# Performance work log

Measured on AMD Instinct MI355X. Metric: run time of the kernel, lower is better.

## Reference

```python
import jax, jax.numpy as jnp
import numpy as np

NP_, NL_, ND_ = 100_000, 10_000, 500
E1, E2 = 2_000_000, 500_000
H, OUT = 128, 10
EPS = 1e-5


def setup_inputs() -> dict:
    key = jax.random.key(0)
    ks = jax.random.split(key, 20)
    n = lambda i, shape, s=1.0: jax.random.normal(ks[i], shape, jnp.float32) * s
    return {
        "x_patient": n(0, (NP_, 16)),
        "x_lab": n(1, (NL_, 1)),
        "x_disease": n(2, (ND_, 2)),
        "Wp": n(3, (16, H), 0.1), "bp": jnp.zeros(H),
        "Wlab": n(4, (1, H), 0.1), "blab": jnp.zeros(H),
        "Wdis": n(5, (2, H), 0.1), "bdis": jnp.zeros(H),
        "Wl1": n(6, (4, H, H), 0.05), "bl1": jnp.zeros((4, H)), "Wr1": n(7, (4, H, H), 0.05),
        "Wl2": n(8, (4, H, H), 0.05), "bl2": jnp.zeros((4, H)), "Wr2": n(9, (4, H, H), 0.05),
        "bn1_g": jnp.ones((3, H)), "bn1_b": jnp.zeros((3, H)),
        "bn2_g": jnp.ones((3, H)), "bn2_b": jnp.zeros((3, H)),
        "fc1_W": n(10, (H, H // 2), 0.1), "fc1_b": jnp.zeros(H // 2),
        "fc2_W": n(11, (H // 2, OUT), 0.1), "fc2_b": jnp.zeros(OUT),
        "e_haslab_src": jax.random.randint(ks[12], (E1,), 0, NP_, jnp.int32),
        "e_haslab_dst": jax.random.randint(ks[13], (E1,), 0, NL_, jnp.int32),
        "e_hasdis_src": jax.random.randint(ks[14], (E2,), 0, NP_, jnp.int32),
        "e_hasdis_dst": jax.random.randint(ks[15], (E2,), 0, ND_, jnp.int32),
    }


def _sage(x_src, x_dst, src, dst, n_dst, Wl, bl, Wr):
    # PyG SAGEConv: lin_l(mean_{j in N(i)} x_j) + lin_r(x_i); bias only on lin_l.
    agg = jax.ops.segment_sum(x_src[src], dst, num_segments=n_dst)  # [n_dst, H]
    cnt = jax.ops.segment_sum(jnp.ones(dst.shape, jnp.float32), dst, num_segments=n_dst)
    mean = agg / jnp.maximum(cnt, 1.0)[:, None]
    return mean @ Wl + bl + x_dst @ Wr


def _bn(x, g, b):
    # training-mode BatchNorm1d (biased variance), eps=1e-5
    m = x.mean(0)
    v = jnp.mean((x - m) ** 2, axis=0)
    return (x - m) * jax.lax.rsqrt(v + EPS) * g + b


def _hetero_layer(hp, hl, hd, s1, d1, s2, d2, Wl, bl, Wr, bn_g, bn_b):
    # edge-type order: 0 has_lab, 1 has_disease, 2 rev_has_lab, 3 rev_has_disease
    out_lab = _sage(hp, hl, s1, d1, NL_, Wl[0], bl[0], Wr[0])
    out_dis = _sage(hp, hd, s2, d2, ND_, Wl[1], bl[1], Wr[1])
    out_pat = (_sage(hl, hp, d1, s1, NP_, Wl[2], bl[2], Wr[2])
               + _sage(hd, hp, d2, s2, NP_, Wl[3], bl[3], Wr[3]))  # HeteroConv aggr='sum'
    hp = jax.nn.relu(_bn(out_pat, bn_g[0], bn_b[0]))
    hl = jax.nn.relu(_bn(out_lab, bn_g[1], bn_b[1]))
    hd = jax.nn.relu(_bn(out_dis, bn_g[2], bn_b[2]))
    return hp, hl, hd


def reference(x_patient, x_lab, x_disease, Wp, bp, Wlab, blab, Wdis, bdis,
              Wl1, bl1, Wr1, Wl2, bl2, Wr2, bn1_g, bn1_b, bn2_g, bn2_b,
              fc1_W, fc1_b, fc2_W, fc2_b,
              e_haslab_src, e_haslab_dst, e_hasdis_src, e_hasdis_dst):
    hp = x_patient @ Wp + bp
    hl = x_lab @ Wlab + blab
    hd = x_disease @ Wdis + bdis
    hp, hl, hd = _hetero_layer(hp, hl, hd, e_haslab_src, e_haslab_dst,
                               e_hasdis_src, e_hasdis_dst, Wl1, bl1, Wr1, bn1_g, bn1_b)
    hp, hl, hd = _hetero_layer(hp, hl, hd, e_haslab_src, e_haslab_dst,
                               e_hasdis_src, e_hasdis_dst, Wl2, bl2, Wr2, bn2_g, bn2_b)
    x = jax.nn.relu(hp @ fc1_W + fc1_b)
    x = x @ fc2_W + fc2_b
    return jax.nn.log_softmax(x, axis=1)
```

## Files before the change

kernel.cpp:

```cpp
#include <hip/hip_runtime.h>
#include <hip/hip_bf16.h>

#define NP 100000
#define NL 10000
#define ND 500
#define H 128
#define HH (H * H)
#define E1 2000000
#define E2 500000
#define EP (E1 + E2)
#define NOUT 10
#define NCNT (NL + ND + 2 * NP)
#define NROW (NL + ND)
#define CHUNK 8192
#define LABHB ((E1 + CHUNK - 1) / CHUNK)
#define DISHB ((E2 + CHUNK - 1) / CHUNK)
#define CNT_BLOCKS ((E1 + E2 + 255) / 256)
#define RED_LAB ((NL + 255) / 256)
#define RED_DIS ((ND + 255) / 256)
#define PAT_BLOCKS (NP / 16)

#define CHP 15625
#define NCH1 (E1 / CHP)
#define NCH2 (E2 / CHP)
#define NPW (NP / 4)
#define RPW ((NPW + 255) / 256)

typedef __hip_bfloat16 bf16;
typedef __attribute__((ext_vector_type(8))) short bf16x8;
typedef __attribute__((ext_vector_type(4))) float f32x4;

__device__ __forceinline__ float bfbits2f(unsigned short s) {
    union { unsigned int u; float f; } v;
    v.u = (unsigned int)s << 16;
    return v.f;
}
__device__ __forceinline__ float2 ld_bf2(const bf16* p) {
    unsigned int u = *(const unsigned int*)p;
    return make_float2(bfbits2f((unsigned short)(u & 0xFFFFu)), bfbits2f((unsigned short)(u >> 16)));
}
__device__ __forceinline__ float2 ld_bf2_nt(const bf16* p) {
    unsigned int u = __builtin_nontemporal_load((const unsigned int*)p);
    return make_float2(bfbits2f((unsigned short)(u & 0xFFFFu)), bfbits2f((unsigned short)(u >> 16)));
}
__device__ __forceinline__ void st_bf2(bf16* p, float2 v) {
    union { unsigned int u; bf16 b[2]; } t;
    t.b[0] = __float2bfloat16(v.x);
    t.b[1] = __float2bfloat16(v.y);
    *(unsigned int*)p = t.u;
}
__device__ __forceinline__ float ldin(const void* p, size_t i, int f32m) {
    return f32m ? ((const float*)p)[i] : __bfloat162float(((const bf16*)p)[i]);
}
__device__ __forceinline__ void bfacc2(float& x, float& y, unsigned int u) {
    union { unsigned int q; float f; } lo, hi;
    lo.q = u << 16;
    hi.q = u & 0xFFFF0000u;
    x += lo.f;
    y += hi.f;
}

#define HB0 NCH1
#define HB1 (HB0 + NCH2)
#define HB2 (HB1 + LABHB)
#define HB3 (HB2 + DISHB)
__global__ void k_hist(const int* __restrict__ e1s, const int* __restrict__ e1d,
                       const int* __restrict__ e2s, const int* __restrict__ e2d,
                       unsigned int* __restrict__ labHistP, unsigned int* __restrict__ disHistP,
                       unsigned char* __restrict__ r1s, unsigned char* __restrict__ r2s,
                       unsigned int* __restrict__ labHist, unsigned int* __restrict__ disHist,
                       const unsigned short* __restrict__ xpw, int* __restrict__ flags) {
    __shared__ unsigned int sh[NPW];
    int b = blockIdx.x, t = threadIdx.x;
    if (b < HB1) {
        for (int i = t; i < NPW; i += 1024) sh[i] = 0;
        __syncthreads();
        if (b < HB0) {
            int e0 = b * CHP;
            for (int j = t; j < CHP; j += 1024) {
                int e = e0 + j;
                int ss = e1s[e];
                unsigned int old = atomicAdd(&sh[ss >> 2], 1u << (8 * (ss & 3)));
                r1s[e] = (unsigned char)(old >> (8 * (ss & 3)));
            }
            __syncthreads();
            unsigned int* out = labHistP + (size_t)b * NPW;
            for (int i = t; i < NPW; i += 1024) out[i] = sh[i];
        } else {
            int c = b - HB0;
            int e0 = c * CHP;
            for (int j = t; j < CHP; j += 1024) {
                int e = e0 + j;
                int ss = e2s[e];
                unsigned int old = atomicAdd(&sh[ss >> 2], 1u << (8 * (ss & 3)));
                r2s[e] = (unsigned char)(old >> (8 * (ss & 3)));
            }
            __syncthreads();
            unsigned int* out = disHistP + (size_t)c * NPW;
            for (int i = t; i < NPW; i += 1024) out[i] = sh[i];
        }
    } else if (b < HB2) {
        int c = b - HB1;
        for (int i = t; i < NL / 2; i += 1024) sh[i] = 0;
        __syncthreads();
        int e0 = c * CHUNK, ee = min(E1, e0 + CHUNK);
        for (int e = e0 + t; e < ee; e += 1024) {
            int dd = e1d[e];
            atomicAdd(&sh[dd >> 1], 1u << (16 * (dd & 1)));
        }
        __syncthreads();
        for (int i = t; i < NL; i += 1024)
            labHist[(size_t)c * NL + i] = (sh[i >> 1] >> (16 * (i & 1))) & 0xFFFFu;
    } else if (b < HB3) {
        int c = b - HB2;
        for (int i = t; i < ND / 2; i += 1024) sh[i] = 0;
        __syncthreads();
        int e0 = c * CHUNK, ee = min(E2, e0 + CHUNK);
        for (int e = e0 + t; e < ee; e += 1024) {
            int dd = e2d[e];
            atomicAdd(&sh[dd >> 1], 1u << (16 * (dd & 1)));
        }
        __syncthreads();
        for (int i = t; i < ND; i += 1024)
            disHist[(size_t)c * ND + i] = (sh[i >> 1] >> (16 * (i & 1))) & 0xFFFFu;
    } else {
        int cnt = 0;
        for (int i = t; i < 4096; i += 1024) {
            unsigned short w = xpw[2 * i];
            int e = (w >> 7) & 0xFF;
            if (w == 0 || (e >= 114 && e <= 141)) cnt++;
        }
        int* shi = (int*)sh;
        shi[t] = cnt;
        __syncthreads();
        for (int s = 512; s > 0; s >>= 1) {
            if (t < s) shi[t] += shi[t + s];
            __syncthreads();
        }
        if (t == 0) flags[0] = (shi[0] < 2048) ? 1 : 0;
    }
}

#define EMB2 ((NP + 255) / 256)
#define RB0 RED_LAB
#define RB1 (RB0 + RED_DIS)
#define RB2 (RB1 + RPW)
#define RB3 (RB2 + RPW)
#define RB4 (RB3 + EMB2)
#define RB5 (RB4 + 16)
#define RB6 (RB5 + 7)
#define RB7 (RB6 + 64)
__global__ void k_reduce(unsigned int* __restrict__ labHist, unsigned int* __restrict__ disHist,
                         unsigned int* __restrict__ labHistP, unsigned int* __restrict__ disHistP,
                         int* __restrict__ cnt, const void* __restrict__ xp,
                         const void* __restrict__ Wp, const void* __restrict__ bp,
                         const void* __restrict__ Wlab, const void* __restrict__ blab,
                         const void* __restrict__ Wdis, const void* __restrict__ bdis,
                         const void* __restrict__ Wl1, const void* __restrict__ bl1,
                         const void* __restrict__ Wr1, bf16* __restrict__ hp,
                         float* __restrict__ WpWl0, float* __restrict__ WpWl1,
                         float* __restrict__ vecs, bf16* __restrict__ w23bT1,
                         bf16* __restrict__ xpb, const int* __restrict__ flags) {
    int b = blockIdx.x, t = threadIdx.x;
    if (b < RB0) {
        int bin = b * 256 + t;
        if (bin < NL) {
            unsigned int run = 0;
            for (int k = 0; k < LABHB; ++k) {
                unsigned int x = labHist[(size_t)k * NL + bin];
                labHist[(size_t)k * NL + bin] = run;
                run += x;
            }
            cnt[bin] = (int)run;
        }
    } else if (b < RB1) {
        int bin = (b - RB0) * 256 + t;
        if (bin < ND) {
            unsigned int run = 0;
            for (int k = 0; k < DISHB; ++k) {
                unsigned int x = disHist[(size_t)k * ND + bin];
                disHist[(size_t)k * ND + bin] = run;
                run += x;
            }
            cnt[NL + bin] = (int)run;
        }
    } else if (b < RB2) {
        int w = (b - RB1) * 256 + t;
        if (w < NPW) {
            unsigned int run = 0;
            for (int c = 0; c < NCH1; ++c) {
                unsigned int x = labHistP[(size_t)c * NPW + w];
                labHistP[(size_t)c * NPW + w] = run;
                run += x;
            }
            int base = NL + ND + 4 * w;
            cnt[base] = (int)(run & 0xFFu);
            cnt[base + 1] = (int)((run >> 8) & 0xFFu);
            cnt[base + 2] = (int)((run >> 16) & 0xFFu);
            cnt[base + 3] = (int)(run >> 24);
        }
    } else if (b < RB3) {
        int w = (b - RB2) * 256 + t;
        if (w < NPW) {
            unsigned int run = 0;
            for (int c = 0; c < NCH2; ++c) {
                unsigned int x = disHistP[(size_t)c * NPW + w];
                disHistP[(size_t)c * NPW + w] = run;
                run += x;
            }
            int base = NL + ND + NP + 4 * w;
            cnt[base] = (int)(run & 0xFFu);
            cnt[base + 1] = (int)((run >> 8) & 0xFFu);
            cnt[base + 2] = (int)((run >> 16) & 0xFFu);
            cnt[base + 3] = (int)(run >> 24);
        }
    } else if (b < RB4) {
        __shared__ float Wps[16 * 128];
        __shared__ float bps[128];
        int f32m = flags[0];
        for (int i = t; i < 16 * 128; i += 256) Wps[i] = ldin(Wp, i, f32m);
        if (t < 128) bps[t] = ldin(bp, t, f32m);
        __syncthreads();
        int p = (b - RB3) * 256 + t;
        if (p < NP) {
            float xr[16];
#pragma unroll
            for (int k = 0; k < 16; ++k) xr[k] = ldin(xp, (size_t)p * 16 + k, f32m);
            unsigned int xw[8];
#pragma unroll
            for (int k2 = 0; k2 < 8; ++k2) {
                union { unsigned int u; bf16 b2[2]; } tt;
                tt.b2[0] = __float2bfloat16(xr[2 * k2]);
                tt.b2[1] = __float2bfloat16(xr[2 * k2 + 1]);
                xw[k2] = tt.u;
            }
            *(uint4*)(xpb + (size_t)p * 16) = make_uint4(xw[0], xw[1], xw[2], xw[3]);
            *(uint4*)(xpb + (size_t)p * 16 + 8) = make_uint4(xw[4], xw[5], xw[6], xw[7]);
            bf16* hrow = hp + (size_t)p * H;
            for (int hc = 0; hc < 16; ++hc) {
                unsigned int ow[4];
#pragma unroll
                for (int hh = 0; hh < 8; hh += 2) {
                    int h0 = hc * 8 + hh;
                    float a0 = bps[h0], a1 = bps[h0 + 1];
#pragma unroll
                    for (int k = 0; k < 16; ++k) {
                        a0 = fmaf(xr[k], Wps[k * 128 + h0], a0);
                        a1 = fmaf(xr[k], Wps[k * 128 + h0 + 1], a1);
                    }
                    union { unsigned int u; bf16 b2[2]; } tt;
                    tt.b2[0] = __float2bfloat16(a0);
                    tt.b2[1] = __float2bfloat16(a1);
                    ow[hh >> 1] = tt.u;
                }
                *(uint4*)(hrow + hc * 8) = make_uint4(ow[0], ow[1], ow[2], ow[3]);
            }
        }
    } else if (b < RB5) {
        int f32m = flags[0];
        int pb = b - RB4;
        bool first = pb < 8;
        size_t woff = first ? 0 : (size_t)HH;
        float* outp = first ? WpWl0 : WpWl1;
        int k = (first ? pb : pb - 8) * 2 + (t >> 7);
        int h = t & 127;
        float s = 0.f;
        for (int m = 0; m < H; ++m)
            s = fmaf(ldin(Wp, (size_t)k * H + m, f32m), ldin(Wl1, woff + (size_t)m * H + h, f32m), s);
        outp[k * H + h] = s;
    } else if (b < RB6) {
        int f32m = flags[0];
        int idx = (b - RB5) * 256 + t;
        if (idx < 13 * 128) {
            int v = idx >> 7, h = idx & 127;
            float s = 0.f;
            if (v == 12) {
                s = ldin(bl1, 2 * H + h, f32m) + ldin(bl1, 3 * H + h, f32m);
            } else {
                const void* A;
                size_t aoff = 0;
                const void* W;
                size_t woff;
                float add = 0.f;
                switch (v) {
                    case 0: A = Wlab; W = Wl1; woff = 2 * (size_t)HH; break;
                    case 1: A = blab; W = Wl1; woff = 2 * (size_t)HH; break;
                    case 2: A = Wdis; W = Wl1; woff = 3 * (size_t)HH; break;
                    case 3: A = Wdis; aoff = H; W = Wl1; woff = 3 * (size_t)HH; break;
                    case 4: A = bdis; W = Wl1; woff = 3 * (size_t)HH; break;
                    case 5: A = Wlab; W = Wr1; woff = 0; break;
                    case 6: A = blab; W = Wr1; woff = 0; add = ldin(bl1, h, f32m); break;
                    case 7: A = Wdis; W = Wr1; woff = (size_t)HH; break;
                    case 8: A = Wdis; aoff = H; W = Wr1; woff = (size_t)HH; break;
                    case 9: A = bdis; W = Wr1; woff = (size_t)HH; add = ldin(bl1, H + h, f32m); break;
                    case 10: A = bp; W = Wl1; woff = 0; break;
                    default: A = bp; W = Wl1; woff = (size_t)HH; break;
                }
                for (int m = 0; m < H; ++m)
                    s = fmaf(ldin(A, aoff + m, f32m), ldin(W, woff + (size_t)m * H + h, f32m), s);
                s += add;
            }
            vecs[v * 128 + h] = s;
        }
    } else {
        int f32m = flags[0];
        int idx = (b - RB6) * 256 + t;
        if (idx < HH) {
            int k = idx >> 7, n = idx & 127;
            float v = ldin(Wr1, (size_t)2 * HH + idx, f32m) + ldin(Wr1, (size_t)3 * HH + idx, f32m);
            w23bT1[(size_t)n * H + k] = __float2bfloat16(v);
        }
    }
}

#define SCAN_ELEMS 2048
__global__ void k_scan1(const int* __restrict__ in, int* __restrict__ out,
                        int* __restrict__ bsums, int n) {
    int t = threadIdx.x;
    int base = blockIdx.x * SCAN_ELEMS + t * 8;
    int v[8], tsum = 0;
#pragma unroll
    for (int j = 0; j < 8; ++j) {
        v[j] = (base + j < n) ? in[base + j] : 0;
        tsum += v[j];
    }
    __shared__ int sh[256];
    sh[t] = tsum;
    __syncthreads();
    for (int d = 1; d < 256; d <<= 1) {
        int x = (t >= d) ? sh[t - d] : 0;
        __syncthreads();
        sh[t] += x;
        __syncthreads();
    }
    int run = sh[t] - tsum;
    if (t == 255) bsums[blockIdx.x] = sh[255];
#pragma unroll
    for (int j = 0; j < 8; ++j) {
        if (base + j < n) out[base + j] = run;
        run += v[j];
    }
}

__global__ void k_scan2(int* __restrict__ bsums, int nb) {
    int t = threadIdx.x;
    int v = (t < nb) ? bsums[t] : 0;
    __shared__ int sh[256];
    sh[t] = v;
    __syncthreads();
    for (int d = 1; d < 256; d <<= 1) {
        int x = (t >= d) ? sh[t - d] : 0;
        __syncthreads();
        sh[t] += x;
        __syncthreads();
    }
    if (t < nb) bsums[t] = sh[t] - v;
}

__global__ void k_scan3(int* __restrict__ out, const int* __restrict__ bsums, int n) {
    int i = blockIdx.x * 256 + threadIdx.x;
    if (i < n) out[i] += bsums[i / SCAN_ELEMS];
}

__global__ void k_fill(const int* __restrict__ e1s, const int* __restrict__ e1d,
                       const int* __restrict__ e2s, const int* __restrict__ e2d,
                       const int* __restrict__ off, const unsigned char* __restrict__ r1s,
                       const unsigned char* __restrict__ r2s,
                       const unsigned char* __restrict__ labBase,
                       const unsigned char* __restrict__ disBase,
                       const unsigned int* __restrict__ labHist,
                       const unsigned int* __restrict__ disHist, int* __restrict__ nbr,
                       unsigned short* __restrict__ nbrP, float* __restrict__ bns) {
    __shared__ unsigned int slot[NL];
    int b = blockIdx.x, t = threadIdx.x;
    if (b < CNT_BLOCKS) {
        int e = b * 256 + t;
        if (e < E1) {
            int ss = e1s[e];
            int c = e / CHP;
            int pos = off[NL + ND + ss] + (int)labBase[(size_t)c * NP + ss] + (int)r1s[e] - EP;
            nbrP[pos] = (unsigned short)e1d[e];
        } else if (e < E1 + E2) {
            int i = e - E1;
            int ss = e2s[i];
            int c = i / CHP;
            int pos = off[NL + ND + NP + ss] + (int)disBase[(size_t)c * NP + ss] + (int)r2s[i] - EP;
            nbrP[pos] = (unsigned short)e2d[i];
        }
    } else if (b < CNT_BLOCKS + LABHB) {
        int c = b - CNT_BLOCKS;
        for (int i = t; i < NL; i += 256)
            slot[i] = (unsigned int)off[i] + labHist[(size_t)c * NL + i];
        __syncthreads();
        int e0 = c * CHUNK, ee = min(E1, e0 + CHUNK);
        for (int e = e0 + t; e < ee; e += 256) {
            unsigned int pos = atomicAdd(&slot[e1d[e]], 1u);
            nbr[pos] = e1s[e];
        }
    } else if (b < CNT_BLOCKS + LABHB + DISHB) {
        int c = b - CNT_BLOCKS - LABHB;
        for (int i = t; i < ND; i += 256)
            slot[i] = (unsigned int)off[NL + i] + disHist[(size_t)c * ND + i];
        __syncthreads();
        int e0 = c * CHUNK, ee = min(E2, e0 + CHUNK);
        for (int e = e0 + t; e < ee; e += 256) {
            unsigned int pos = atomicAdd(&slot[e2d[e]], 1u);
            nbr[pos] = e2s[e];
        }
    } else {
        for (int i = t; i < 8 * H; i += 256) bns[i] = 0.f;
    }
}

__global__ void k_stage1_L1(const bf16* __restrict__ xpb, const int* __restrict__ off,
                            const int* __restrict__ cnt, const int* __restrict__ nbr,
                            float* __restrict__ mxp) {
    __shared__ float red[4][64][16];
    int t = threadIdx.x;
    int w = t >> 6, lane = t & 63;
    int row = blockIdx.x * 4 + w;
    float acc[16];
#pragma unroll
    for (int d = 0; d < 16; ++d) acc[d] = 0.f;
    if (row < NROW) {
        int s0 = off[row], c = cnt[row];
        const int* nb = nbr + s0;
        int j = lane;
        for (; j + 64 < c; j += 128) {
            int p0 = nb[j], p1 = nb[j + 64];
            const uint4* r0 = (const uint4*)(xpb + (size_t)p0 * 16);
            const uint4* r1 = (const uint4*)(xpb + (size_t)p1 * 16);
            uint4 u0 = r0[0], u1 = r0[1];
            uint4 v0 = r1[0], v1 = r1[1];
            bfacc2(acc[0], acc[1], u0.x);   bfacc2(acc[2], acc[3], u0.y);
            bfacc2(acc[4], acc[5], u0.z);   bfacc2(acc[6], acc[7], u0.w);
            bfacc2(acc[8], acc[9], u1.x);   bfacc2(acc[10], acc[11], u1.y);
            bfacc2(acc[12], acc[13], u1.z); bfacc2(acc[14], acc[15], u1.w);
            bfacc2(acc[0], acc[1], v0.x);   bfacc2(acc[2], acc[3], v0.y);
            bfacc2(acc[4], acc[5], v0.z);   bfacc2(acc[6], acc[7], v0.w);
            bfacc2(acc[8], acc[9], v1.x);   bfacc2(acc[10], acc[11], v1.y);
            bfacc2(acc[12], acc[13], v1.z); bfacc2(acc[14], acc[15], v1.w);
        }
        if (j < c) {
            const uint4* r0 = (const uint4*)(xpb + (size_t)nb[j] * 16);
            uint4 u0 = r0[0], u1 = r0[1];
            bfacc2(acc[0], acc[1], u0.x);   bfacc2(acc[2], acc[3], u0.y);
            bfacc2(acc[4], acc[5], u0.z);   bfacc2(acc[6], acc[7], u0.w);
            bfacc2(acc[8], acc[9], u1.x);   bfacc2(acc[10], acc[11], u1.y);
            bfacc2(acc[12], acc[13], u1.z); bfacc2(acc[14], acc[15], u1.w);
        }
    }
#pragma unroll
    for (int d = 0; d < 16; ++d) red[w][lane][d] = acc[d];
    __syncthreads();
    if (t < 64) {
        int w2 = t >> 4, d = t & 15;
        int row2 = blockIdx.x * 4 + w2;
        if (row2 < NROW) {
            float s = 0.f;
#pragma unroll 8
            for (int l = 0; l < 64; ++l) s += red[w2][l][d];
            mxp[(size_t)row2 * 16 + d] = s / fmaxf((float)cnt[row2], 1.f);
        }
    }
}

#define LD1_BLOCKS ((NROW + 1) / 2)
#define HPAD 136
#define APAD 132
__global__ void k_patmm_L1(const bf16* __restrict__ hp, const void* __restrict__ xl,
                           const void* __restrict__ xd, const int* __restrict__ off,
                           const int* __restrict__ cnt, const unsigned short* __restrict__ nbrP,
                           const bf16* __restrict__ w23bT1, const float* __restrict__ vecs,
                           const float* __restrict__ WpWl0, const float* __restrict__ WpWl1,
                           const float* __restrict__ mxp, bf16* __restrict__ aggp,
                           float* __restrict__ bufL, float* __restrict__ bufD,
                           float* __restrict__ blocksums, const int* __restrict__ flags) {
    int t = threadIdx.x;
    int f32m = flags[0];
    if (blockIdx.x < PAT_BLOCKS) {
        __shared__ bf16 hpA[16][HPAD];
        __shared__ float accf[16][APAD];
        __shared__ float svec[6][128];
        __shared__ float s_mxl[16], s_onL[16], s_d0[16], s_d1[16], s_onD[16];
        int w = t >> 6, lane = t & 63;
        int p0 = blockIdx.x * 16;
        {
            const unsigned int* hpu = (const unsigned int*)(hp + (size_t)p0 * H);
            for (int i = t; i < 16 * 64; i += 256) {
                int r = i >> 6, c = i & 63;
                *(unsigned int*)&hpA[r][2 * c] = hpu[(size_t)r * 64 + c];
            }
        }
        {
            const int map[6] = {0, 1, 2, 3, 4, 12};
            for (int i = t; i < 6 * 128; i += 256)
                svec[i >> 7][i & 127] = vecs[map[i >> 7] * 128 + (i & 127)];
        }
        {
            int g = t >> 4, sl = t & 15;
            int p = p0 + g;
            int s1 = off[NL + ND + p] - EP, c1 = cnt[NL + ND + p];
            float a = 0.f;
            for (int j = sl; j < c1; j += 16) a += ldin(xl, nbrP[s1 + j], f32m);
            a += __shfl_xor(a, 1);
            a += __shfl_xor(a, 2);
            a += __shfl_xor(a, 4);
            a += __shfl_xor(a, 8);
            int s2 = off[NL + ND + NP + p] - EP, c2 = cnt[NL + ND + NP + p];
            float d0 = 0.f, d1 = 0.f;
            for (int j = sl; j < c2; j += 16) {
                int q = nbrP[s2 + j];
                d0 += ldin(xd, (size_t)2 * q, f32m);
                d1 += ldin(xd, (size_t)2 * q + 1, f32m);
            }
            d0 += __shfl_xor(d0, 1); d0 += __shfl_xor(d0, 2);
            d0 += __shfl_xor(d0, 4); d0 += __shfl_xor(d0, 8);
            d1 += __shfl_xor(d1, 1); d1 += __shfl_xor(d1, 2);
            d1 += __shfl_xor(d1, 4); d1 += __shfl_xor(d1, 8);
            if (sl == 0) {
                s_mxl[g] = a / fmaxf((float)c1, 1.f);
                s_onL[g] = (c1 > 0) ? 1.f : 0.f;
                s_d0[g] = d0 / fmaxf((float)c2, 1.f);
                s_d1[g] = d1 / fmaxf((float)c2, 1.f);
                s_onD[g] = (c2 > 0) ? 1.f : 0.f;
            }
        }
        __syncthreads();
        {
            int m = lane & 15, kg = lane >> 4;
            bf16x8 afr[4];
#pragma unroll
            for (int ks = 0; ks < 4; ++ks)
                afr[ks] = *(const bf16x8*)&hpA[m][ks * 32 + kg * 8];
            int n0 = w * 32;
#pragma unroll
            for (int tt = 0; tt < 2; ++tt) {
                int nc = n0 + tt * 16 + m;
                f32x4 acc = {0.f, 0.f, 0.f, 0.f};
#pragma unroll
                for (int ks = 0; ks < 4; ++ks) {
                    bf16x8 bfr = *(const bf16x8*)&w23bT1[(size_t)nc * H + ks * 32 + kg * 8];
                    acc = __builtin_amdgcn_mfma_f32_16x16x32_bf16(afr[ks], bfr, acc, 0, 0, 0);
                }
#pragma unroll
                for (int rg = 0; rg < 4; ++rg)
                    accf[kg * 4 + rg][nc] = acc[rg];
            }
        }
        __syncthreads();
        for (int i = t; i < 16 * 64; i += 256) {
            int r = i >> 6, cc = (i & 63) * 2;
            float l0 = s_onL[r] * fmaf(s_mxl[r], svec[0][cc], svec[1][cc]);
            float l1 = s_onL[r] * fmaf(s_mxl[r], svec[0][cc + 1], svec[1][cc + 1]);
            float q0 = s_onD[r] * (s_d0[r] * svec[2][cc] + s_d1[r] * svec[3][cc] + svec[4][cc]);
            float q1 = s_onD[r] * (s_d0[r] * svec[2][cc + 1] + s_d1[r] * svec[3][cc + 1] + svec[4][cc + 1]);
            float v0 = accf[r][cc] + l0 + q0 + svec[5][cc];
            float v1 = accf[r][cc + 1] + l1 + q1 + svec[5][cc + 1];
            accf[r][cc] = v0;
            accf[r][cc + 1] = v1;
            st_bf2(aggp + (size_t)(p0 + r) * H + cc, make_float2(v0, v1));
        }
        __syncthreads();
        if (t < 128) {
            float s = 0.f, q = 0.f;
#pragma unroll
            for (int r = 0; r < 16; ++r) {
                float v = accf[r][t];
                s += v;
                q = fmaf(v, v, q);
            }
            blocksums[(size_t)blockIdx.x * 256 + t] = s;
            blocksums[(size_t)blockIdx.x * 256 + 128 + t] = q;
        }
    } else {
        int bb = blockIdx.x - PAT_BLOCKS;
        int rr = bb * 2 + (t >> 7);
        int h = t & 127;
        if (rr >= NROW) return;
        if (rr < NL) {
            float acc = vecs[6 * 128 + h] + ldin(xl, rr, f32m) * vecs[5 * 128 + h];
            if (cnt[rr] > 0) {
                float s = vecs[10 * 128 + h];
                const float* mx = mxp + (size_t)rr * 16;
#pragma unroll
                for (int k = 0; k < 16; ++k) s = fmaf(mx[k], WpWl0[k * H + h], s);
                acc += s;
            }
            bufL[(size_t)rr * H + h] = acc;
        } else {
            int rd = rr - NL;
            float acc = vecs[9 * 128 + h] + ldin(xd, (size_t)2 * rd, f32m) * vecs[7 * 128 + h] +
                        ldin(xd, (size_t)2 * rd + 1, f32m) * vecs[8 * 128 + h];
            if (cnt[rr] > 0) {
                float s = vecs[11 * 128 + h];
                const float* mx = mxp + (size_t)rr * 16;
#pragma unroll
                for (int k = 0; k < 16; ++k) s = fmaf(mx[k], WpWl1[k * H + h], s);
                acc += s;
            }
            bufD[(size_t)rd * H + h] = acc;
        }
    }
}

__global__ void k_bnred(const float* __restrict__ blocksums, const float* __restrict__ bufL,
                        const float* __restrict__ bufD, float* __restrict__ sums) {
    int b = blockIdx.x, t = threadIdx.x;
    if (b < 64) {
        float acc = 0.f;
        for (int r = b; r < PAT_BLOCKS; r += 64) acc += blocksums[(size_t)r * 256 + t];
        atomicAdd(&sums[t], acc);
        return;
    }
    int h = t & 127;
    int sub = t >> 7;
    float s = 0.f, s2 = 0.f;
    float* sm;
    if (b < 320) {
        int bid = b - 64;
        for (int i = bid * 2 + sub; i < NL; i += 512) {
            float v = bufL[(size_t)i * H + h];
            s += v;
            s2 = fmaf(v, v, s2);
        }
        sm = sums + 2 * H;
    } else {
        int bid = b - 320;
        for (int i = bid * 2 + sub; i < ND; i += 128) {
            float v = bufD[(size_t)i * H + h];
            s += v;
            s2 = fmaf(v, v, s2);
        }
        sm = sums + 4 * H;
    }
    __shared__ float ls[256], ls2[256];
    ls[t] = s;
    ls2[t] = s2;
    __syncthreads();
    if (sub == 0) {
        atomicAdd(&sm[h], s + ls[128 + h]);
        atomicAdd(&sm[H + h], s2 + ls2[128 + h]);
    }
}

#define S2_MM 1313
#define S2_PREP 64
#define S2_TOTAL (S2_MM + S2_PREP)
__global__ void k_stage1_L2(const float* __restrict__ bufL, const float* __restrict__ bufD,
                            const float* __restrict__ bns, const void* __restrict__ bng1,
                            const void* __restrict__ bnb1, const void* __restrict__ Wl,
                            bf16* __restrict__ tlp, bf16* __restrict__ tdp,
                            const void* __restrict__ Wr, const void* __restrict__ bl,
                            bf16* __restrict__ w23bT, float* __restrict__ b23,
                            const void* __restrict__ W1in, bf16* __restrict__ w1T,
                            const int* __restrict__ flags) {
    __shared__ float smm[8][H];
    int b = blockIdx.x, t = threadIdx.x;
    int f32m = flags[0];
    if (b < S2_MM) {
        int bb = b;
        bool lab = bb < 1250;
        const float* buf = lab ? bufL : bufD;
        int N = lab ? NL : ND;
        float invN = lab ? 1.f / NL : 1.f / ND;
        int so = lab ? 2 * H : 4 * H;
        int go = lab ? H : 2 * H;
        bf16* outp = lab ? tlp : tdp;
        size_t woff = lab ? (size_t)2 * HH : (size_t)3 * HH;
        int r0 = (lab ? bb : bb - 1250) * 8;
        int h = t & 127, half = t >> 7;
        float m = bns[so + h] * invN;
        float v = fmaf(-m, m, bns[so + H + h] * invN);
        float sc = rsqrtf(v + 1e-5f) * ldin(bng1, go + h, f32m);
        float be = ldin(bnb1, go + h, f32m);
        for (int r = half; r < 8; r += 2) {
            int ri = r0 + r;
            float x = (ri < N) ? buf[(size_t)ri * H + h] : 0.f;
            smm[r][h] = (ri < N) ? fmaxf(fmaf(x - m, sc, be), 0.f) : 0.f;
        }
        __syncthreads();
        int rb = half * 4;
        float a0 = 0.f, a1 = 0.f, a2 = 0.f, a3 = 0.f;
        for (int k = 0; k < H; ++k) {
            float wv = ldin(Wl, woff + (size_t)k * H + h, f32m);
            a0 = fmaf(smm[rb + 0][k], wv, a0);
            a1 = fmaf(smm[rb + 1][k], wv, a1);
            a2 = fmaf(smm[rb + 2][k], wv, a2);
            a3 = fmaf(smm[rb + 3][k], wv, a3);
        }
        float acc[4] = {a0, a1, a2, a3};
#pragma unroll
        for (int r = 0; r < 4; ++r)
            if (r0 + rb + r < N)
                outp[(size_t)(r0 + rb + r) * H + h] = __float2bfloat16(acc[r]);
    } else {
        int pb = b - S2_MM;
        int idx = pb * 256 + t;
        if (idx < HH) {
            int k = idx >> 7, n = idx & 127;
            float v = ldin(Wr, (size_t)2 * HH + idx, f32m) + ldin(Wr, (size_t)3 * HH + idx, f32m);
            w23bT[(size_t)n * H + k] = __float2bfloat16(v);
        }
        if (idx < H)
            b23[idx] = ldin(bl, (size_t)2 * H + idx, f32m) + ldin(bl, (size_t)3 * H + idx, f32m);
        if (idx < 64 * H) {
            int n = idx >> 7, k = idx & 127;
            w1T[idx] = __float2bfloat16(ldin(W1in, (size_t)k * 64 + n, f32m));
        }
    }
}

__global__ void k_patmm_L2(bf16* __restrict__ aggp, const bf16* __restrict__ tlp,
                           const bf16* __restrict__ tdp, const int* __restrict__ off,
                           const int* __restrict__ cnt, const unsigned short* __restrict__ nbrP,
                           const bf16* __restrict__ w23bT, const float* __restrict__ b23,
                           const float* __restrict__ bns, const void* __restrict__ bng1,
                           const void* __restrict__ bnb1, float* __restrict__ blocksums,
                           const int* __restrict__ flags) {
    __shared__ bf16 hpA[16][HPAD];
    __shared__ __align__(16) float accf[16][APAD];
    int t = threadIdx.x;
    int f32m = flags[0];
    int w = t >> 6, lane = t & 63;
    int p0 = blockIdx.x * 16;
    {
        int cc = (t & 63) * 2;
        const float invN = 1.f / NP;
        float m0 = bns[cc] * invN, m1 = bns[cc + 1] * invN;
        float v0 = fmaf(-m0, m0, bns[128 + cc] * invN);
        float v1 = fmaf(-m1, m1, bns[128 + cc + 1] * invN);
        float sc0 = rsqrtf(v0 + 1e-5f) * ldin(bng1, cc, f32m);
        float sc1 = rsqrtf(v1 + 1e-5f) * ldin(bng1, cc + 1, f32m);
        float be0 = ldin(bnb1, cc, f32m), be1 = ldin(bnb1, cc + 1, f32m);
        for (int i = t; i < 16 * 64; i += 256) {
            int r = i >> 6;
            float2 v = ld_bf2_nt(aggp + (size_t)(p0 + r) * H + cc);
            st_bf2(&hpA[r][cc], make_float2(fmaxf(fmaf(v.x - m0, sc0, be0), 0.f),
                                            fmaxf(fmaf(v.y - m1, sc1, be1), 0.f)));
        }
    }
    {
        const int* off1 = off + NL + ND;
        const int* cnt1 = cnt + NL + ND;
        const int* off2 = off + NL + ND + NP;
        const int* cnt2 = cnt + NL + ND + NP;
        int qw = lane >> 4, ql = lane & 15;
        int p = p0 + w * 4 + qw;
        int cb = ql * 8;
        float4 bb0 = *(const float4*)(b23 + cb);
        float4 bb1 = *(const float4*)(b23 + cb + 4);
        int s1 = off1[p] - EP, c1 = cnt1[p];
        const unsigned short* nb1 = nbrP + s1;
        float a0 = 0.f, a1 = 0.f, a2 = 0.f, a3 = 0.f, a4 = 0.f, a5 = 0.f, a6 = 0.f, a7 = 0.f;
        float g0 = 0.f, g1 = 0.f, g2 = 0.f, g3 = 0.f, g4 = 0.f, g5 = 0.f, g6 = 0.f, g7 = 0.f;
        int j = 0;
        int i0, i1, i2, i3;
        if (c1 >= 4) { i0 = nb1[0]; i1 = nb1[1]; i2 = nb1[2]; i3 = nb1[3]; }
        for (; j + 8 <= c1; j += 4) {
            uint4 v0 = *(const uint4*)(tlp + (size_t)i0 * H + cb);
            uint4 v1 = *(const uint4*)(tlp + (size_t)i1 * H + cb);
            uint4 v2 = *(const uint4*)(tlp + (size_t)i2 * H + cb);
            uint4 v3 = *(const uint4*)(tlp + (size_t)i3 * H + cb);
            int n0 = nb1[j + 4], n1 = nb1[j + 5], n2 = nb1[j + 6], n3 = nb1[j + 7];
            bfacc2(a0, a1, v0.x); bfacc2(a2, a3, v0.y); bfacc2(a4, a5, v0.z); bfacc2(a6, a7, v0.w);
            bfacc2(g0, g1, v1.x); bfacc2(g2, g3, v1.y); bfacc2(g4, g5, v1.z); bfacc2(g6, g7, v1.w);
            bfacc2(a0, a1, v2.x); bfacc2(a2, a3, v2.y); bfacc2(a4, a5, v2.z); bfacc2(a6, a7, v2.w);
            bfacc2(g0, g1, v3.x); bfacc2(g2, g3, v3.y); bfacc2(g4, g5, v3.z); bfacc2(g6, g7, v3.w);
            i0 = n0; i1 = n1; i2 = n2; i3 = n3;
        }
        if (j + 4 <= c1) {
            uint4 v0 = *(const uint4*)(tlp + (size_t)i0 * H + cb);
            uint4 v1 = *(const uint4*)(tlp + (size_t)i1 * H + cb);
            uint4 v2 = *(const uint4*)(tlp + (size_t)i2 * H + cb);
            uint4 v3 = *(const uint4*)(tlp + (size_t)i3 * H + cb);
            bfacc2(a0, a1, v0.x); bfacc2(a2, a3, v0.y); bfacc2(a4, a5, v0.z); bfacc2(a6, a7, v0.w);
            bfacc2(g0, g1, v1.x); bfacc2(g2, g3, v1.y); bfacc2(g4, g5, v1.z); bfacc2(g6, g7, v1.w);
            bfacc2(a0, a1, v2.x); bfacc2(a2, a3, v2.y); bfacc2(a4, a5, v2.z); bfacc2(a6, a7, v2.w);
            bfacc2(g0, g1, v3.x); bfacc2(g2, g3, v3.y); bfacc2(g4, g5, v3.z); bfacc2(g6, g7, v3.w);
            j += 4;
        }
        for (; j < c1; ++j) {
            uint4 v = *(const uint4*)(tlp + (size_t)nb1[j] * H + cb);
            bfacc2(a0, a1, v.x); bfacc2(a2, a3, v.y); bfacc2(a4, a5, v.z); bfacc2(a6, a7, v.w);
        }
        a0 += g0; a1 += g1; a2 += g2; a3 += g3;
        a4 += g4; a5 += g5; a6 += g6; a7 += g7;
        int s2 = off2[p] - EP, c2 = cnt2[p];
        const unsigned short* nb2 = nbrP + s2;
        float d0 = 0.f, d1 = 0.f, d2 = 0.f, d3 = 0.f, d4 = 0.f, d5 = 0.f, d6 = 0.f, d7 = 0.f;
        float e0 = 0.f, e1 = 0.f, e2 = 0.f, e3 = 0.f, e4 = 0.f, e5 = 0.f, e6 = 0.f, e7 = 0.f;
        j = 0;
        int k0, k1;
        if (c2 >= 2) { k0 = nb2[0]; k1 = nb2[1]; }
        for (; j + 4 <= c2; j += 2) {
            uint4 v0 = *(const uint4*)(tdp + (size_t)k0 * H + cb);
            uint4 v1 = *(const uint4*)(tdp + (size_t)k1 * H + cb);
            int n0 = nb2[j + 2], n1 = nb2[j + 3];
            bfacc2(d0, d1, v0.x); bfacc2(d2, d3, v0.y); bfacc2(d4, d5, v0.z); bfacc2(d6, d7, v0.w);
            bfacc2(e0, e1, v1.x); bfacc2(e2, e3, v1.y); bfacc2(e4, e5, v1.z); bfacc2(e6, e7, v1.w);
            k0 = n0; k1 = n1;
        }
        if (j + 2 <= c2) {
            uint4 v0 = *(const uint4*)(tdp + (size_t)k0 * H + cb);
            uint4 v1 = *(const uint4*)(tdp + (size_t)k1 * H + cb);
            bfacc2(d0, d1, v0.x); bfacc2(d2, d3, v0.y); bfacc2(d4, d5, v0.z); bfacc2(d6, d7, v0.w);
            bfacc2(e0, e1, v1.x); bfacc2(e2, e3, v1.y); bfacc2(e4, e5, v1.z); bfacc2(e6, e7, v1.w);
            j += 2;
        }
        if (j < c2) {
            uint4 v = *(const uint4*)(tdp + (size_t)nb2[j] * H + cb);
            bfacc2(d0, d1, v.x); bfacc2(d2, d3, v.y); bfacc2(d4, d5, v.z); bfacc2(d6, d7, v.w);
        }
        d0 += e0; d1 += e1; d2 += e2; d3 += e3;
        d4 += e4; d5 += e5; d6 += e6; d7 += e7;
        float i1f = 1.f / fmaxf((float)c1, 1.f), i2f = 1.f / fmaxf((float)c2, 1.f);
        float4 r0v, r1v;
        r0v.x = a0 * i1f + d0 * i2f + bb0.x;
        r0v.y = a1 * i1f + d1 * i2f + bb0.y;
        r0v.z = a2 * i1f + d2 * i2f + bb0.z;
        r0v.w = a3 * i1f + d3 * i2f + bb0.w;
        r1v.x = a4 * i1f + d4 * i2f + bb1.x;
        r1v.y = a5 * i1f + d5 * i2f + bb1.y;
        r1v.z = a6 * i1f + d6 * i2f + bb1.z;
        r1v.w = a7 * i1f + d7 * i2f + bb1.w;
        *(float4*)&accf[w * 4 + qw][cb] = r0v;
        *(float4*)&accf[w * 4 + qw][cb + 4] = r1v;
    }
    __syncthreads();
    {
        int m = lane & 15, kg = lane >> 4;
        bf16x8 afr[4];
#pragma unroll
        for (int ks = 0; ks < 4; ++ks)
            afr[ks] = *(const bf16x8*)&hpA[m][ks * 32 + kg * 8];
        int n0 = w * 32;
#pragma unroll
        for (int tt = 0; tt < 2; ++tt) {
            int nc = n0 + tt * 16 + m;
            f32x4 acc = {0.f, 0.f, 0.f, 0.f};
#pragma unroll
            for (int ks = 0; ks < 4; ++ks) {
                bf16x8 bfr = *(const bf16x8*)&w23bT[(size_t)nc * H + ks * 32 + kg * 8];
                acc = __builtin_amdgcn_mfma_f32_16x16x32_bf16(afr[ks], bfr, acc, 0, 0, 0);
            }
#pragma unroll
            for (int rg = 0; rg < 4; ++rg)
                accf[kg * 4 + rg][nc] += acc[rg];
        }
    }
    __syncthreads();
    for (int i = t; i < 16 * 64; i += 256) {
        int r = i >> 6, cc = (i & 63) * 2;
        st_bf2(aggp + (size_t)(p0 + r) * H + cc, make_float2(accf[r][cc], accf[r][cc + 1]));
    }
    if (t < 128) {
        float s = 0.f, q = 0.f;
#pragma unroll
        for (int r = 0; r < 16; ++r) {
            float v = accf[r][t];
            s += v;
            q = fmaf(v, v, q);
        }
        blocksums[(size_t)blockIdx.x * 256 + t] = s;
        blocksums[(size_t)blockIdx.x * 256 + 128 + t] = q;
    }
}

__global__ void k_head(const bf16* __restrict__ aggp, const float* __restrict__ sums,
                       const void* __restrict__ bng, const void* __restrict__ bnb,
                       const bf16* __restrict__ w1T, const void* __restrict__ b1,
                       const void* __restrict__ W2, const void* __restrict__ b2f,
                       void* __restrict__ out, const int* __restrict__ flags) {
    int f32m = flags[0];
    __shared__ bf16 hpA[16][HPAD];
    __shared__ float h1s[16][68];
    __shared__ float lgs[16][16];
    __shared__ float W2s[64 * NOUT];
    __shared__ float b1s[64], b2s[NOUT];
    int t = threadIdx.x;
    int w = t >> 6, lane = t & 63;
    for (int i = t; i < 64 * NOUT; i += 256) W2s[i] = ldin(W2, i, f32m);
    if (t < 64) b1s[t] = ldin(b1, t, f32m);
    else if (t >= 64 && t < 64 + NOUT) b2s[t - 64] = ldin(b2f, t - 64, f32m);
    int p0 = blockIdx.x * 16;
    {
        int cc = (t & 63) * 2;
        const float invN = 1.f / NP;
        float m0 = sums[cc] * invN, m1 = sums[cc + 1] * invN;
        float v0 = fmaf(-m0, m0, sums[128 + cc] * invN);
        float v1 = fmaf(-m1, m1, sums[128 + cc + 1] * invN);
        float sc0 = rsqrtf(v0 + 1e-5f) * ldin(bng, cc, f32m);
        float sc1 = rsqrtf(v1 + 1e-5f) * ldin(bng, cc + 1, f32m);
        float be0 = ldin(bnb, cc, f32m), be1 = ldin(bnb, cc + 1, f32m);
        for (int i = t; i < 16 * 64; i += 256) {
            int r = i >> 6;
            float2 v = ld_bf2_nt(aggp + (size_t)(p0 + r) * H + cc);
            st_bf2(&hpA[r][cc], make_float2(fmaxf(fmaf(v.x - m0, sc0, be0), 0.f),
                                            fmaxf(fmaf(v.y - m1, sc1, be1), 0.f)));
        }
    }
    __syncthreads();
    {
        int m = lane & 15, kg = lane >> 4;
        bf16x8 afr[4];
#pragma unroll
        for (int ks = 0; ks < 4; ++ks)
            afr[ks] = *(const bf16x8*)&hpA[m][ks * 32 + kg * 8];
        int nc = w * 16 + m;
        f32x4 acc = {0.f, 0.f, 0.f, 0.f};
#pragma unroll
        for (int ks = 0; ks < 4; ++ks) {
            bf16x8 bfr = *(const bf16x8*)&w1T[(size_t)nc * H + ks * 32 + kg * 8];
            acc = __builtin_amdgcn_mfma_f32_16x16x32_bf16(afr[ks], bfr, acc, 0, 0, 0);
        }
        float bv = b1s[nc];
#pragma unroll
        for (int rg = 0; rg < 4; ++rg)
            h1s[kg * 4 + rg][nc] = fmaxf(acc[rg] + bv, 0.f);
    }
    __syncthreads();
    int pat = lane >> 4, oidx = lane & 15;
    int prow = 4 * w + pat;
    float lg = 0.f;
    if (oidx < NOUT) {
        lg = b2s[oidx];
        const float* hh = h1s[prow];
#pragma unroll 8
        for (int k = 0; k < 64; ++k) lg = fmaf(hh[k], W2s[k * NOUT + oidx], lg);
        lgs[prow][oidx] = lg;
    }
    __syncthreads();
    if (oidx < NOUT) {
        float m = -1e30f;
#pragma unroll
        for (int k = 0; k < NOUT; ++k) m = fmaxf(m, lgs[prow][k]);
        float s = 0.f;
#pragma unroll
        for (int k = 0; k < NOUT; ++k) s += __expf(lgs[prow][k] - m);
        float r = lg - m - __logf(s);
        if (f32m)
            ((float*)out)[(size_t)(p0 + prow) * NOUT + oidx] = r;
        else
            ((bf16*)out)[(size_t)(p0 + prow) * NOUT + oidx] = __float2bfloat16(r);
    }
}

extern "C" void kernel_launch(void* const* d_in, const int* in_sizes, int n_in, void* d_out,
                              int out_size, void* d_ws, size_t ws_size, hipStream_t stream) {
    const int* e1s = (const int*)d_in[23];
    const int* e1d = (const int*)d_in[24];
    const int* e2s = (const int*)d_in[25];
    const int* e2d = (const int*)d_in[26];

    char* wsb = (char*)d_ws;
    size_t o = 0;
    auto af = [&](size_t nwords) { void* p = wsb + o * 4; o += nwords; return p; };
    int* flags = (int*)af(16);
    bf16* w23bT = (bf16*)af(HH / 2);
    bf16* w23bT1 = (bf16*)af(HH / 2);
    bf16* w1T = (bf16*)af(64 * H / 2);
    float* b23 = (float*)af(H);
    float* bns = (float*)af(8 * H);
    int* bsums = (int*)af(256);
    float* WpWl0 = (float*)af(16 * H);
    float* WpWl1 = (float*)af(16 * H);
    float* vecs = (float*)af(13 * 128);
    int* cnt = (int*)af(NCNT);
    int* off = (int*)af(NCNT);
    int* nbr = (int*)af(EP);
    unsigned short* nbrP = (unsigned short*)af(EP / 2);
    bf16* hp = (bf16*)af((size_t)NP * H / 2);
    bf16* xpb = (bf16*)af((size_t)NP * 16 / 2);
    size_t arena = o;
    unsigned char* r1s = (unsigned char*)af(E1 / 4);
    unsigned char* r2s = (unsigned char*)af(E2 / 4);
    unsigned int* labHistP = (unsigned int*)af((size_t)NCH1 * NPW);
    unsigned int* disHistP = (unsigned int*)af((size_t)NCH2 * NPW);
    unsigned int* labHist = (unsigned int*)af((size_t)LABHB * NL);
    unsigned int* disHist = (unsigned int*)af((size_t)DISHB * ND);
    size_t endA = o;
    o = arena;
    float* bufL = (float*)af((size_t)NL * H);
    float* bufD = (float*)af((size_t)ND * H);
    bf16* tlp = (bf16*)af((size_t)NL * H / 2);
    bf16* tdp = (bf16*)af((size_t)ND * H / 2);
    bf16* aggp = (bf16*)af((size_t)NP * H / 2);
    float* mxp = (float*)af((size_t)NROW * 16);
    float* blocksums = (float*)af((size_t)PAT_BLOCKS * 256);
    size_t endB = o;
    o = endA > endB ? endA : endB;
    (void)ws_size;

    k_hist<<<HB3 + 1, 1024, 0, stream>>>(e1s, e1d, e2s, e2d, labHistP, disHistP, r1s, r2s,
                                         labHist, disHist, (const unsigned short*)d_in[0],
                                         flags);
    k_reduce<<<RB7, 256, 0, stream>>>(labHist, disHist, labHistP, disHistP, cnt, d_in[0],
                                      d_in[3], d_in[4], d_in[5], d_in[6], d_in[7], d_in[8],
                                      d_in[9], d_in[10], d_in[11], hp, WpWl0, WpWl1, vecs,
                                      w23bT1, xpb, flags);
    int nb = (NCNT + SCAN_ELEMS - 1) / SCAN_ELEMS;
    k_scan1<<<nb, 256, 0, stream>>>(cnt, off, bsums, NCNT);
    k_scan2<<<1, 256, 0, stream>>>(bsums, nb);
    k_scan3<<<(NCNT + 255) / 256, 256, 0, stream>>>(off, bsums, NCNT);
    k_fill<<<CNT_BLOCKS + LABHB + DISHB + 1, 256, 0, stream>>>(
        e1s, e1d, e2s, e2d, off, r1s, r2s, (const unsigned char*)labHistP,
        (const unsigned char*)disHistP, labHist, disHist, nbr, nbrP, bns);

    k_stage1_L1<<<(NROW + 3) / 4, 256, 0, stream>>>(xpb, off, cnt, nbr, mxp);
    k_patmm_L1<<<PAT_BLOCKS + LD1_BLOCKS, 256, 0, stream>>>(hp, d_in[1], d_in[2], off, cnt,
                                                            nbrP, w23bT1, vecs, WpWl0, WpWl1,
                                                            mxp, aggp, bufL, bufD, blocksums,
                                                            flags);
    k_bnred<<<384, 256, 0, stream>>>(blocksums, bufL, bufD, bns);

    k_stage1_L2<<<S2_TOTAL, 256, 0, stream>>>(bufL, bufD, bns, d_in[15], d_in[16], d_in[12],
                                              tlp, tdp, d_in[14], d_in[13], w23bT, b23,
                                              d_in[19], w1T, flags);
    k_patmm_L2<<<PAT_BLOCKS, 256, 0, stream>>>(aggp, tlp, tdp, off, cnt, nbrP, w23bT, b23, bns,
                                               d_in[15], d_in[16], blocksums, flags);
    k_bnred<<<64, 256, 0, stream>>>(blocksums, bufL, bufD, bns + 6 * H);
    k_head<<<NP / 16, 256, 0, stream>>>(aggp, bns + 6 * H, d_in[17], d_in[18], w1T,
                                        d_in[20], d_in[21], d_in[22], d_out, flags);
}
```

Measured before the change: 538.5 us.

## Partition CSR fill by destination range across XCD-strided blocks

Rewrites k_fill so that each group of 8 blocks splits the destination id space into 8 ranges. Each block scans its edge chunk and writes only edges whose target falls in its range. The likely intent is to keep the scattered writes and the per-row lookups (off, labBase) for one range inside a single XCD's L2, and to cut the LDS slot array from NL to NL/8 entries. The cost is that every edge index is now read 8 times, and there are more blocks doing filtered loops.

```diff
diff --git a/kernel.cpp b/kernel.cpp
--- a/kernel.cpp
+++ b/kernel.cpp
@@ -15,7 +15,6 @@
 #define CHUNK 8192
 #define LABHB ((E1 + CHUNK - 1) / CHUNK)
 #define DISHB ((E2 + CHUNK - 1) / CHUNK)
-#define CNT_BLOCKS ((E1 + E2 + 255) / 256)
 #define RED_LAB ((NL + 255) / 256)
 #define RED_DIS ((ND + 255) / 256)
 #define PAT_BLOCKS (NP / 16)
@@ -25,6 +24,16 @@
 #define NCH2 (E2 / CHP)
 #define NPW (NP / 4)
 #define RPW ((NPW + 255) / 256)
+
+#define NPG 256
+#define PB_P (8 * NPG)
+#define S1E ((E1 + NPG - 1) / NPG)
+#define S2E ((E2 + NPG - 1) / NPG)
+#define PB_L (8 * LABHB)
+#define PB_D (8 * DISHB)
+#define NLR (NL / 8)
+#define NDR 63
+#define NPR 12500
 
 typedef __hip_bfloat16 bf16;
 typedef __attribute__((ext_vector_type(8))) short bf16x8;
@@ -371,44 +380,65 @@
                        const unsigned int* __restrict__ labHist,
                        const unsigned int* __restrict__ disHist, int* __restrict__ nbr,
                        unsigned short* __restrict__ nbrP, float* __restrict__ bns) {
-    __shared__ unsigned int slot[NL];
+    __shared__ unsigned int slot[NLR];
     int b = blockIdx.x, t = threadIdx.x;
-    if (b < CNT_BLOCKS) {
-        int e = b * 256 + t;
-        if (e < E1) {
-            int ss = e1s[e];
-            int c = e / CHP;
-            int pos = off[NL + ND + ss] + (int)labBase[(size_t)c * NP + ss] + (int)r1s[e] - EP;
-            nbrP[pos] = (unsigned short)e1d[e];
-        } else if (e < E1 + E2) {
-            int i = e - E1;
-            int ss = e2s[i];
-            int c = i / CHP;
-            int pos = off[NL + ND + NP + ss] + (int)disBase[(size_t)c * NP + ss] + (int)r2s[i] - EP;
-            nbrP[pos] = (unsigned short)e2d[i];
-        }
-    } else if (b < CNT_BLOCKS + LABHB) {
-        int c = b - CNT_BLOCKS;
-        for (int i = t; i < NL; i += 256)
-            slot[i] = (unsigned int)off[i] + labHist[(size_t)c * NL + i];
+    if (b < PB_P) {
+        int x = b & 7, g = b >> 3;
+        unsigned int lo = (unsigned int)x * NPR;
+        int e0 = g * S1E, ee = min(E1, e0 + S1E);
+        for (int e = e0 + t; e < ee; e += 256) {
+            unsigned int ss = (unsigned int)e1s[e];
+            if (ss - lo < (unsigned int)NPR) {
+                int c = e / CHP;
+                int pos = off[NL + ND + ss] + (int)labBase[(size_t)c * NP + ss] + (int)r1s[e] - EP;
+                nbrP[pos] = (unsigned short)e1d[e];
+            }
+        }
+        e0 = g * S2E; ee = min(E2, e0 + S2E);
+        for (int e = e0 + t; e < ee; e += 256) {
+            unsigned int ss = (unsigned int)e2s[e];
+            if (ss - lo < (unsigned int)NPR) {
+                int c = e / CHP;
+                int pos = off[NL + ND + NP + ss] + (int)disBase[(size_t)c * NP + ss] + (int)r2s[e] - EP;
+                nbrP[pos] = (unsigned short)e2d[e];
+            }
+        }
+    } else if (b < PB_P + PB_L) {
+        int idx = b - PB_P;
+        int x = idx & 7, c = idx >> 3;
+        int lo = x * NLR;
+        for (int i = t; i < NLR; i += 256)
+            slot[i] = (unsigned int)off[lo + i] + labHist[(size_t)c * NL + lo + i];
         __syncthreads();
         int e0 = c * CHUNK, ee = min(E1, e0 + CHUNK);
         for (int e = e0 + t; e < ee; e += 256) {
-            unsigned int pos = atomicAdd(&slot[e1d[e]], 1u);
-            nbr[pos] = e1s[e];
-        }
-    } else if (b < CNT_BLOCKS + LABHB + DISHB) {
-        int c = b - CNT_BLOCKS - LABHB;
-        for (int i = t; i < ND; i += 256)
-            slot[i] = (unsigned int)off[NL + i] + disHist[(size_t)c * ND + i];
+            unsigned int dd = (unsigned int)e1d[e];
+            if (dd - (unsigned int)lo < (unsigned int)NLR) {
+                unsigned int pos = atomicAdd(&slot[dd - lo], 1u);
+                nbr[pos] = e1s[e];
+            }
+        }
+    } else if (b < PB_P + PB_L + PB_D) {
+        int idx = b - PB_P - PB_L;
+        int x = idx & 7, c = idx >> 3;
+        int lo = x * NDR;
+        int nr = ND - lo;
+        if (nr > NDR) nr = NDR;
+        if (nr < 0) nr = 0;
+        for (int i = t; i < nr; i += 256)
+            slot[i] = (unsigned int)off[NL + lo + i] + disHist[(size_t)c * ND + lo + i];
         __syncthreads();
         int e0 = c * CHUNK, ee = min(E2, e0 + CHUNK);
         for (int e = e0 + t; e < ee; e += 256) {
-            unsigned int pos = atomicAdd(&slot[e2d[e]], 1u);
-            nbr[pos] = e2s[e];
+            unsigned int dd = (unsigned int)e2d[e];
+            if (dd - (unsigned int)lo < (unsigned int)nr) {
+                unsigned int pos = atomicAdd(&slot[dd - lo], 1u);
+                nbr[pos] = e2s[e];
+            }
         }
     } else {
-        for (int i = t; i < 8 * H; i += 256) bns[i] = 0.f;
+        int bb = b - PB_P - PB_L - PB_D;
+        for (int i = t; i < H; i += 256) bns[bb * H + i] = 0.f;
     }
 }
 
@@ -1003,7 +1033,7 @@
     k_scan1<<<nb, 256, 0, stream>>>(cnt, off, bsums, NCNT);
     k_scan2<<<1, 256, 0, stream>>>(bsums, nb);
     k_scan3<<<(NCNT + 255) / 256, 256, 0, stream>>>(off, bsums, NCNT);
-    k_fill<<<CNT_BLOCKS + LABHB + DISHB + 1, 256, 0, stream>>>(
+    k_fill<<<PB_P + PB_L + PB_D + 8, 256, 0, stream>>>(
         e1s, e1d, e2s, e2d, off, r1s, r2s, (const unsigned char*)labHistP,
         (const unsigned char*)disHistP, labHist, disHist, nbr, nbrP, bns);
 
```

After: 552.0 us. +2.5%, slower.
